# Optimization experiments

Measured on AMD Instinct MI355X. Metric: run time of the kernel, lower is better.

The kernel has to match this reference:

```python
import jax, jax.numpy as jnp
import numpy as np

B, L, H, D, T = 8, 4096, 8, 128, 128  # batch, max_len, kv_heads, head_size, max_new_tokens


def setup_inputs() -> dict:
    key = jax.random.key(0)
    ks = jax.random.split(key, 6)
    return {
        "keys": jax.random.normal(ks[0], (B, L, H, D), dtype=jnp.float32),
        "values": jax.random.normal(ks[1], (B, L, H, D), dtype=jnp.float32),
        "lengths": jax.random.randint(ks[2], (B,), 0, 2048, dtype=jnp.int32),
        "new_keys": jax.random.normal(ks[3], (B, T, H, D), dtype=jnp.float32),
        "new_values": jax.random.normal(ks[4], (B, T, H, D), dtype=jnp.float32),
        "new_lengths": jax.random.randint(ks[5], (B,), 0, T, dtype=jnp.int32),
    }


def reference(keys, values, lengths, new_keys, new_values, new_lengths):
    max_new_tokens = new_values.shape[1]
    max_len = keys.shape[1]
    operands = (keys, values, lengths, new_keys, new_values, new_lengths)

    def specialized_path(ops):
        k, v, l, nk, nv, nl = ops
        batch_size = k.shape[0]
        batch_idx = jnp.arange(batch_size)
        pos_idx = l
        update_vals_k = nk[:, 0]
        update_vals_v = nv[:, 0]
        should_update = (nl == 1)[:, None, None]
        original_vals_k = k[batch_idx, pos_idx]
        original_vals_v = v[batch_idx, pos_idx]
        vals_to_set_k = jnp.where(should_update, update_vals_k, original_vals_k)
        vals_to_set_v = jnp.where(should_update, update_vals_v, original_vals_v)
        updated_k = k.at[batch_idx, pos_idx].set(vals_to_set_k)
        updated_v = v.at[batch_idx, pos_idx].set(vals_to_set_v)
        return (updated_k, updated_v)

    def general_path(ops):
        k, v, l, nk, nv, nl = ops
        batch_size = k.shape[0]
        b_coords, p_coords = jnp.indices((batch_size, max_len))
        lengths_b = l[:, None]
        new_lengths_b = nl[:, None]
        update_mask = (p_coords >= lengths_b) & (p_coords < lengths_b + new_lengths_b)
        source_indices = p_coords - lengths_b
        clipped_source_indices = jnp.clip(source_indices, 0, max_new_tokens - 1)
        values_to_write_k = nk[b_coords, clipped_source_indices]
        values_to_write_v = nv[b_coords, clipped_source_indices]
        broadcast_mask = update_mask[:, :, None, None]
        updated_k = jnp.where(broadcast_mask, values_to_write_k, k)
        updated_v = jnp.where(broadcast_mask, values_to_write_v, v)
        return (updated_k, updated_v)

    is_special_case = jnp.all(new_lengths <= 1)
    updated_keys, updated_values = jax.lax.cond(is_special_case, specialized_path, general_path, operands)
    updated_lengths = lengths + new_lengths
    return (updated_keys, updated_values, updated_lengths)
```

## Files before the change

kernel.cpp:

```cpp
#include <hip/hip_runtime.h>

constexpr int B = 8;
constexpr int L = 4096;
constexpr int H = 8;
constexpr int D = 128;
constexpr int T = 128;

constexpr long long KV_ELEMS = (long long)B * L * H * D;
constexpr int TOTAL4 = (int)(KV_ELEMS / 4);

constexpr int NBLOCKS = 2048;
constexpr int NTHREADS = 256;
constexpr int STRIDE = NBLOCKS * NTHREADS;

typedef float f4 __attribute__((ext_vector_type(4)));

__global__ __launch_bounds__(256) void kv_fused_phased(
    const f4* __restrict__ keys,
    const f4* __restrict__ values,
    const int* __restrict__ lengths,
    const f4* __restrict__ new_keys,
    const f4* __restrict__ new_values,
    const int* __restrict__ new_lengths,
    f4* __restrict__ out_k,
    f4* __restrict__ out_v,
    float* __restrict__ out_len)
{
    const int tid = blockIdx.x * NTHREADS + (int)threadIdx.x;

    #pragma unroll 1
    for (int it = 0; it < 32; ++it) {
        const bool is_k = (it < 16);
        const f4* __restrict__ src  = is_k ? keys     : values;
        const f4* __restrict__ nsrc = is_k ? new_keys : new_values;
        f4* __restrict__ dst        = is_k ? out_k    : out_v;

        const int i = (it & 15) * STRIDE + tid;

        f4 v = __builtin_nontemporal_load(&src[i]);

        const int row = i >> 8;
        const int b   = row >> 12;
        const int p   = row & (L - 1);
        const int l   = lengths[b];
        const int nl  = new_lengths[b];

        if (p >= l && p < l + nl) {
            const int c    = i & 255;
            const int nidx = ((b * T + (p - l)) << 8) + c;
            v = nsrc[nidx];
        }

        __builtin_nontemporal_store(v, &dst[i]);
    }

    if (blockIdx.x == 0 && threadIdx.x < B) {
        const int bb = threadIdx.x;
        out_len[bb] = (float)(lengths[bb] + new_lengths[bb]);
    }
}

extern "C" void kernel_launch(void* const* d_in, const int* in_sizes, int n_in,
                              void* d_out, int out_size, void* d_ws, size_t ws_size,
                              hipStream_t stream)
{
    const f4* keys        = (const f4*)d_in[0];
    const f4* values      = (const f4*)d_in[1];
    const int* lengths    = (const int*)d_in[2];
    const f4* new_keys    = (const f4*)d_in[3];
    const f4* new_values  = (const f4*)d_in[4];
    const int* new_lengths= (const int*)d_in[5];

    float* out     = (float*)d_out;
    f4* out_k      = (f4*)out;
    f4* out_v      = (f4*)(out + KV_ELEMS);
    float* out_len = out + 2 * KV_ELEMS;

    kv_fused_phased<<<NBLOCKS, NTHREADS, 0, stream>>>(keys, values, lengths,
                                                      new_keys, new_values, new_lengths,
                                                      out_k, out_v, out_len);
}
```

Baseline: 96.96 us.

## Split fused KV update into plain bulk copies plus scatter patch kernel

Replaces the single fused kernel, which checked the update window per element, with two pure nontemporal copy kernels (keys, values) and a small patch kernel that writes only the new-token rows afterwards. This drops the per-element lengths lookup and branch from the bandwidth-bound copy loop. In exchange it adds two extra kernel launches, and the patch kernel rewrites rows already written by the copies, relying on stream ordering for correctness.

```diff
diff --git a/kernel.cpp b/kernel.cpp
--- a/kernel.cpp
+++ b/kernel.cpp
@@ -15,43 +15,36 @@
 
 typedef float f4 __attribute__((ext_vector_type(4)));
 
-__global__ __launch_bounds__(256) void kv_fused_phased(
-    const f4* __restrict__ keys,
-    const f4* __restrict__ values,
-    const int* __restrict__ lengths,
+__global__ __launch_bounds__(256) void kv_copy_nt(
+    const f4* __restrict__ src,
+    f4* __restrict__ dst)
+{
+    int i = blockIdx.x * NTHREADS + (int)threadIdx.x;
+    #pragma unroll 1
+    for (int it = 0; it < 16; ++it, i += STRIDE) {
+        __builtin_nontemporal_store(__builtin_nontemporal_load(&src[i]), &dst[i]);
+    }
+}
+
+__global__ __launch_bounds__(256) void kv_patch(
     const f4* __restrict__ new_keys,
     const f4* __restrict__ new_values,
+    const int* __restrict__ lengths,
     const int* __restrict__ new_lengths,
     f4* __restrict__ out_k,
     f4* __restrict__ out_v,
     float* __restrict__ out_len)
 {
-    const int tid = blockIdx.x * NTHREADS + (int)threadIdx.x;
+    const int b = blockIdx.x >> 7;
+    const int t = blockIdx.x & (T - 1);
 
-    #pragma unroll 1
-    for (int it = 0; it < 32; ++it) {
-        const bool is_k = (it < 16);
-        const f4* __restrict__ src  = is_k ? keys     : values;
-        const f4* __restrict__ nsrc = is_k ? new_keys : new_values;
-        f4* __restrict__ dst        = is_k ? out_k    : out_v;
-
-        const int i = (it & 15) * STRIDE + tid;
-
-        f4 v = __builtin_nontemporal_load(&src[i]);
-
-        const int row = i >> 8;
-        const int b   = row >> 12;
-        const int p   = row & (L - 1);
-        const int l   = lengths[b];
-        const int nl  = new_lengths[b];
-
-        if (p >= l && p < l + nl) {
-            const int c    = i & 255;
-            const int nidx = ((b * T + (p - l)) << 8) + c;
-            v = nsrc[nidx];
-        }
-
-        __builtin_nontemporal_store(v, &dst[i]);
+    if (t < new_lengths[b]) {
+        const int l = lengths[b];
+        const int c = threadIdx.x;
+        const int srci = ((b * T + t) << 8) + c;
+        const int dsti = ((b * L + l + t) << 8) + c;
+        out_k[dsti] = new_keys[srci];
+        out_v[dsti] = new_values[srci];
     }
 
     if (blockIdx.x == 0 && threadIdx.x < B) {
@@ -76,7 +69,10 @@
     f4* out_v      = (f4*)(out + KV_ELEMS);
     float* out_len = out + 2 * KV_ELEMS;
 
-    kv_fused_phased<<<NBLOCKS, NTHREADS, 0, stream>>>(keys, values, lengths,
-                                                      new_keys, new_values, new_lengths,
-                                                      out_k, out_v, out_len);
+    kv_copy_nt<<<NBLOCKS, NTHREADS, 0, stream>>>(keys,   out_k);
+    kv_copy_nt<<<NBLOCKS, NTHREADS, 0, stream>>>(values, out_v);
+
+    kv_patch<<<B * T, NTHREADS, 0, stream>>>(new_keys, new_values,
+                                             lengths, new_lengths,
+                                             out_k, out_v, out_len);
 }
```

Result: slower. 100.9 us (+4.1%).
